# Kernel tuning notes

Hardware: AMD Instinct MI355X
Metric: run time of the kernel (lower is better)

## Reference

```python
import jax, jax.numpy as jnp
import numpy as np
import math

B, S, H = 8, 1024, 1024
NUM_LABELS = 2

# torch nn.Linear weight [out,in]; we store transposed [in,out] so y = x @ W + b

def _mha(x, mask, qw, qb, kw, kb, vw, vb, ow, ob, n_heads):
    b, s, h = x.shape
    d = h // n_heads
    Q = (x @ qw + qb).reshape(b, s, n_heads, d)
    K = (x @ kw + kb).reshape(b, s, n_heads, d)
    V = (x @ vw + vb).reshape(b, s, n_heads, d)
    scores = jnp.einsum('bqhd,bkhd->bhqk', Q, K) / math.sqrt(d)  # [b,h,s,s]
    if mask is not None:
        scores = jnp.where(mask[:, None, None, :] == 0, jnp.asarray(-1e9, scores.dtype), scores)
    w = jax.nn.softmax(scores, axis=-1)  # dropout is identity in eval mode
    ctx = jnp.einsum('bhqk,bkhd->bqhd', w, V).reshape(b, s, h)
    return ctx @ ow + ob, w


def _linear_params(key, fin, fout):
    k1, k2 = jax.random.split(key)
    lim = 1.0 / math.sqrt(fin)
    w = jax.random.uniform(k1, (fin, fout), jnp.float32, -lim, lim)
    b = jax.random.uniform(k2, (fout,), jnp.float32, -lim, lim)
    return w, b


def setup_inputs() -> dict:
    key = jax.random.key(0)
    ks = jax.random.split(key, 20)
    inp = {
        'hidden_states': jax.random.normal(ks[0], (B, S, H), jnp.float32),
        'attention_mask': jax.random.randint(ks[1], (B, S), 0, 2, jnp.int32),
    }
    i = 2
    for pre in ('beh', 'tmp', 'pat'):
        for nm in ('q', 'k', 'v', 'o'):
            w, b = _linear_params(ks[i], H, H)
            inp[f'{pre}_{nm}w'] = w
            inp[f'{pre}_{nm}b'] = b
            i += 1
    inp['fus1_w'], inp['fus1_b'] = _linear_params(ks[i], 3 * H, H); i += 1
    inp['fus2_w'], inp['fus2_b'] = _linear_params(ks[i], H, H // 2); i += 1
    inp['cls_w'], inp['cls_b'] = _linear_params(ks[i], H // 2, NUM_LABELS)
    return inp


def reference(hidden_states, attention_mask,
              beh_qw, beh_qb, beh_kw, beh_kb, beh_vw, beh_vb, beh_ow, beh_ob,
              tmp_qw, tmp_qb, tmp_kw, tmp_kb, tmp_vw, tmp_vb, tmp_ow, tmp_ob,
              pat_qw, pat_qb, pat_kw, pat_kb, pat_vw, pat_vb, pat_ow, pat_ob,
              fus1_w, fus1_b, fus2_w, fus2_b, cls_w, cls_b):
    beh_out, _ = _mha(hidden_states, attention_mask, beh_qw, beh_qb, beh_kw, beh_kb, beh_vw, beh_vb, beh_ow, beh_ob, 8)
    tmp_out, _ = _mha(hidden_states, attention_mask, tmp_qw, tmp_qb, tmp_kw, tmp_kb, tmp_vw, tmp_vb, tmp_ow, tmp_ob, 4)
    pat_out, _ = _mha(hidden_states, attention_mask, pat_qw, pat_qb, pat_kw, pat_kb, pat_vw, pat_vb, pat_ow, pat_ob, 4)
    m = attention_mask[:, :, None].astype(hidden_states.dtype)  # [B,S,1]
    denom = m.sum(axis=1)  # [B,1] broadcast like torch expand_as sum
    beh_p = (beh_out * m).sum(axis=1) / denom
    tmp_p = (tmp_out * m).sum(axis=1) / denom
    pat_p = (pat_out * m).sum(axis=1) / denom
    fused = jnp.concatenate([beh_p, tmp_p, pat_p], axis=-1)  # [B,3H]
    h1 = jax.nn.relu(fused @ fus1_w + fus1_b)
    h2 = jax.nn.relu(h1 @ fus2_w + fus2_b)
    logits = h2 @ cls_w + cls_b
    return logits
```

## Files before the change

### kernel.cpp

```cpp
#include <hip/hip_runtime.h>

#define DEVINL __device__ __forceinline__
typedef __attribute__((ext_vector_type(8))) __bf16 bf16x8;
typedef __attribute__((ext_vector_type(4))) __bf16 bf16x4;
typedef __attribute__((ext_vector_type(4))) float f32x4;

DEVINL void gload16(void* lds, const void* g) {
  __builtin_amdgcn_global_load_lds((const __attribute__((address_space(1))) void*)g,
                                   (__attribute__((address_space(3))) void*)lds, 16, 0, 0);
}

__global__ void cvt_bf16_kernel(const float* __restrict__ in, __bf16* __restrict__ out, int n4) {
  int i = blockIdx.x * 256 + threadIdx.x;
  if (i >= n4) return;
  float4 v = reinterpret_cast<const float4*>(in)[i];
  bf16x4 o;
  o.x = (__bf16)v.x; o.y = (__bf16)v.y; o.z = (__bf16)v.z; o.w = (__bf16)v.w;
  reinterpret_cast<bf16x4*>(out)[i] = o;
}

__global__ void wt_pack_kernel(const float* __restrict__ Wq, const float* __restrict__ Wk,
                               const float* __restrict__ Wv, __bf16* __restrict__ WT) {
  __shared__ float t[64][65];
  int k0 = blockIdx.x * 64;
  int n0 = blockIdx.y * 64;
  const float* W = (n0 < 1024) ? Wq : (n0 < 2048 ? Wk : Wv);
  int nn0 = n0 & 1023;
  int r = threadIdx.x >> 6, c = threadIdx.x & 63;
#pragma unroll
  for (int i = 0; i < 16; ++i)
    t[r + i*4][c] = W[(size_t)(k0 + r + i*4) * 1024 + nn0 + c];
  __syncthreads();
#pragma unroll
  for (int i = 0; i < 16; ++i) {
    int row = r + i*4;
    WT[(size_t)(n0 + row) * 1024 + k0 + c] = (__bf16)t[c][row];
  }
}

__global__ __launch_bounds__(256) void gemm_qkv_kernel(
    const __bf16* __restrict__ A, const __bf16* __restrict__ WT,
    const float* __restrict__ bq, const float* __restrict__ bk, const float* __restrict__ bv,
    __bf16* __restrict__ C) {
  constexpr int N_ = 3072, K_ = 1024;
  __shared__ __align__(16) __bf16 lds[2][(128 + 128) * 64];
  int tid = threadIdx.x;
  int lane = tid & 63;
  int wave = tid >> 6;
  int l15 = lane & 15, l4 = lane >> 4;
  int wr = wave >> 1, wc = wave & 1;
  int n0 = blockIdx.x * 128, m0 = blockIdx.y * 128;

  f32x4 acc[4][4] = {};

  const char* Abase = (const char*)(A  + (size_t)m0 * K_);
  const char* Bbase = (const char*)(WT + (size_t)n0 * K_);

  auto STAGE = [&](int buf, int kt) {
    char* Al = (char*)lds[buf];
    char* Bl = (char*)(lds[buf] + 128 * 64);
#pragma unroll
    for (int i = 0; i < 4; ++i) {
      int c = i * 256 + tid;
      int r = c >> 3, cc = c & 7, g = cc ^ (r & 7);
      gload16(Al + (size_t)(c & ~63) * 16,
              Abase + (size_t)r * (K_ * 2) + kt * 128 + g * 16);
      gload16(Bl + (size_t)(c & ~63) * 16,
              Bbase + (size_t)r * (K_ * 2) + kt * 128 + g * 16);
    }
  };

  int cur = 0;
  STAGE(0, 0);
  for (int kt = 0; kt < 16; ++kt) {
    if (kt < 15) {
      STAGE(cur ^ 1, kt + 1);
      asm volatile("s_waitcnt vmcnt(8)" ::: "memory");
    } else {
      asm volatile("s_waitcnt vmcnt(0)" ::: "memory");
    }
    __builtin_amdgcn_s_barrier();
    const char* Al = (const char*)lds[cur];
    const char* Bl = (const char*)(lds[cur] + 128 * 64);
#pragma unroll
    for (int kk = 0; kk < 2; ++kk) {
      bf16x8 af[4], bfr[4];
      int j = kk * 4 + l4;
#pragma unroll
      for (int m = 0; m < 4; ++m) {
        int row = wr * 64 + m * 16 + l15;
        af[m] = *(const bf16x8*)(Al + ((size_t)row * 8 + (j ^ (row & 7))) * 16);
      }
#pragma unroll
      for (int n = 0; n < 4; ++n) {
        int row = wc * 64 + n * 16 + l15;
        bfr[n] = *(const bf16x8*)(Bl + ((size_t)row * 8 + (j ^ (row & 7))) * 16);
      }
      __builtin_amdgcn_s_setprio(1);
#pragma unroll
      for (int m = 0; m < 4; ++m)
#pragma unroll
        for (int n = 0; n < 4; ++n)
          acc[m][n] = __builtin_amdgcn_mfma_f32_16x16x32_bf16(af[m], bfr[n], acc[m][n], 0, 0, 0);
      __builtin_amdgcn_s_setprio(0);
    }
    __builtin_amdgcn_s_barrier();
    cur ^= 1;
  }

#pragma unroll
  for (int n = 0; n < 4; ++n) {
    int col = n0 + wc * 64 + n * 16 + l15;
    const float* bias = (col < 1024) ? bq : (col < 2048 ? bk : bv);
    float bv_ = bias[col & 1023];
#pragma unroll
    for (int m = 0; m < 4; ++m) {
      int rowb = m0 + wr * 64 + m * 16 + l4 * 4;
#pragma unroll
      for (int r = 0; r < 4; ++r)
        C[(size_t)(rowb + r) * N_ + col] = (__bf16)(acc[m][n][r] + bv_);
    }
  }
}

__global__ void vt_pack_kernel(const __bf16* __restrict__ QKV, __bf16* __restrict__ Vt,
                               int hcnt, int D) {
  __shared__ __bf16 t[64][65];
  int s0 = blockIdx.x * 64, d0 = blockIdx.y * 64;
  int bh = blockIdx.z;
  int b = bh / hcnt, h = bh - b*hcnt;
  int r = threadIdx.x >> 6, c = threadIdx.x & 63;
  const __bf16* src = QKV + (size_t)b*1024*3072 + 2048 + (size_t)h*D;
#pragma unroll
  for (int i = 0; i < 16; ++i)
    t[r + i*4][c] = src[(size_t)(s0 + r + i*4)*3072 + d0 + c];
  __syncthreads();
  __bf16* dst = Vt + ((size_t)bh*D + d0)*1024 + s0;
#pragma unroll
  for (int i = 0; i < 16; ++i) {
    int row = r + i*4;
    dst[(size_t)row*1024 + c] = t[c][row];
  }
}

template<int D, int WQ, int HCNT>
__global__ __launch_bounds__(256) void attn_kernel(
    const __bf16* __restrict__ QKV, const __bf16* __restrict__ Vt,
    const int* __restrict__ mask, float* __restrict__ ctx) {
  constexpr int QT  = 4*WQ;
  constexpr int MT  = WQ/16;
  constexpr int KC  = D/32;
  constexpr int NT2 = D/16;
  constexpr int CPR = D/8;
  __shared__ __align__(16) __bf16 smem[64*D + D*64 + 4*WQ*72];
  __shared__ float Ml[64];
  __bf16* Kl = smem;
  __bf16* Vl = smem + 64*D;
  __bf16* Pl = smem + 128*D;

  int tid = threadIdx.x;
  int lane = tid & 63, wave = tid >> 6;
  int l15 = lane & 15, l4 = lane >> 4;
  int q0 = blockIdx.x * QT;
  int h = blockIdx.y, b = blockIdx.z;
  int bh = b*HCNT + h;
  const float scale = (D == 128) ? 0.08838834764831845f : 0.0625f;

  {
    const char* qbase = (const char*)(QKV + (size_t)(b*1024 + q0)*3072 + (size_t)h*D);
    for (int c0 = 0; c0 < QT*D/8; c0 += 256) {
      int c = c0 + tid;
      int row = c / CPR, cc = c % CPR;
      gload16((char*)smem + (c0 + (tid & ~63))*16,
              qbase + (size_t)row*6144 + ((cc ^ (row & 7))*16));
    }
  }
  __syncthreads();
  bf16x8 qf[MT][KC];
#pragma unroll
  for (int m = 0; m < MT; ++m)
#pragma unroll
    for (int kc = 0; kc < KC; ++kc) {
      int row = wave*WQ + m*16 + l15;
      int boff = ((kc*32 + l4*8)*2) ^ ((row & 7) << 4);
      qf[m][kc] = *(const bf16x8*)((const char*)smem + (size_t)row*(D*2) + boff);
    }
  __syncthreads();

  f32x4 ao[MT][NT2] = {};
  float dsum[MT][4] = {};

  const char* kbase = (const char*)(QKV + (size_t)(b*1024)*3072 + 1024 + (size_t)h*D);
  const char* vbase = (const char*)(Vt + (size_t)bh*D*1024);

  for (int t = 0; t < 16; ++t) {
    for (int c0 = 0; c0 < 8*D; c0 += 256) {
      int c = c0 + tid;
      int row = c / CPR, cc = c % CPR;
      gload16((char*)Kl + (c0 + (tid & ~63))*16,
              kbase + (size_t)(t*64 + row)*6144 + ((cc ^ (row & 7))*16));
    }
    for (int c0 = 0; c0 < 8*D; c0 += 256) {
      int c = c0 + tid;
      int row = c >> 3, cc = c & 7;
      gload16((char*)Vl + (c0 + (tid & ~63))*16,
              vbase + (size_t)row*2048 + t*128 + ((cc ^ (row & 7))*16));
    }
    if (tid < 64) Ml[tid] = (float)mask[b*1024 + t*64 + tid];
    __syncthreads();

#pragma unroll
    for (int n = 0; n < 4; ++n) {
      f32x4 s[MT] = {};
#pragma unroll
      for (int kc = 0; kc < KC; ++kc) {
        int krow = n*16 + l15;
        int boff = ((kc*32 + l4*8)*2) ^ ((krow & 7) << 4);
        bf16x8 kf = *(const bf16x8*)((const char*)Kl + (size_t)krow*(D*2) + boff);
#pragma unroll
        for (int m = 0; m < MT; ++m)
          s[m] = __builtin_amdgcn_mfma_f32_16x16x32_bf16(qf[m][kc], kf, s[m], 0, 0, 0);
      }
      float mv = Ml[n*16 + l15];
#pragma unroll
      for (int m = 0; m < MT; ++m)
#pragma unroll
        for (int r = 0; r < 4; ++r) {
          float pf_ = __expf(s[m][r] * scale) * mv;
          __bf16 pb = (__bf16)pf_;
          dsum[m][r] += (float)pb;
          Pl[(size_t)(wave*WQ + m*16 + l4*4 + r)*72 + n*16 + l15] = pb;
        }
    }
    bf16x8 pfr[MT][2];
#pragma unroll
    for (int m = 0; m < MT; ++m)
#pragma unroll
      for (int kk = 0; kk < 2; ++kk)
        pfr[m][kk] = *(const bf16x8*)(Pl + (size_t)(wave*WQ + m*16 + l15)*72 + kk*32 + l4*8);
#pragma unroll
    for (int n2 = 0; n2 < NT2; ++n2) {
      bf16x8 vf[2];
#pragma unroll
      for (int kk = 0; kk < 2; ++kk) {
        int vrow = n2*16 + l15;
        int boff = ((kk*32 + l4*8)*2) ^ ((vrow & 7) << 4);
        vf[kk] = *(const bf16x8*)((const char*)Vl + (size_t)vrow*128 + boff);
      }
#pragma unroll
      for (int m = 0; m < MT; ++m)
#pragma unroll
        for (int kk = 0; kk < 2; ++kk)
          ao[m][n2] = __builtin_amdgcn_mfma_f32_16x16x32_bf16(pfr[m][kk], vf[kk], ao[m][n2], 0, 0, 0);
    }
    __syncthreads();
  }

  float inv[MT][4];
#pragma unroll
  for (int m = 0; m < MT; ++m)
#pragma unroll
    for (int r = 0; r < 4; ++r) {
      float v = dsum[m][r];
      v += __shfl_xor(v, 1, 64);
      v += __shfl_xor(v, 2, 64);
      v += __shfl_xor(v, 4, 64);
      v += __shfl_xor(v, 8, 64);
      inv[m][r] = 1.0f / v;
    }
#pragma unroll
  for (int m = 0; m < MT; ++m) {
    int rowb = b*1024 + q0 + wave*WQ + m*16 + l4*4;
#pragma unroll
    for (int n2 = 0; n2 < NT2; ++n2) {
      int col = h*D + n2*16 + l15;
#pragma unroll
      for (int r = 0; r < 4; ++r)
        ctx[(size_t)(rowb + r)*1024 + col] = ao[m][n2][r] * inv[m][r];
    }
  }
}

__global__ void denom_kernel(const int* __restrict__ mask, float* __restrict__ denom) {
  int b = blockIdx.x, t = threadIdx.x;
  int acc = 0;
  for (int s = t; s < 1024; s += 256) acc += mask[b*1024 + s];
  for (int o = 32; o; o >>= 1) acc += __shfl_down(acc, o, 64);
  __shared__ int red[4];
  if ((t & 63) == 0) red[t >> 6] = acc;
  __syncthreads();
  if (t == 0) denom[b] = (float)(red[0] + red[1] + red[2] + red[3]);
}

__global__ void pool_partial_kernel(const float* __restrict__ ctx, const int* __restrict__ mask,
                                    float* __restrict__ part) {
  int sc = blockIdx.x;
  int b  = blockIdx.y;
  int t  = threadIdx.x;
  const float* base = ctx + (size_t)b*1024*1024 + (size_t)sc*32*1024;
  const int* mrow = mask + b*1024 + sc*32;
  float4 acc = {0.f, 0.f, 0.f, 0.f};
  for (int s = 0; s < 32; ++s) {
    if (mrow[s]) {
      float4 v = reinterpret_cast<const float4*>(base + (size_t)s*1024)[t];
      acc.x += v.x; acc.y += v.y; acc.z += v.z; acc.w += v.w;
    }
  }
  reinterpret_cast<float4*>(part + ((size_t)b*32 + sc)*1024)[t] = acc;
}

__global__ void pool_reduce_kernel(const float* __restrict__ part, const float* __restrict__ denom,
                                   float* __restrict__ out) {
  int i = blockIdx.x*256 + threadIdx.x;
  int b = i >> 10, c = i & 1023;
  float a = 0.f;
#pragma unroll
  for (int sc = 0; sc < 32; ++sc) a += part[((size_t)b*32 + sc)*1024 + c];
  out[i] = a / denom[b];
}

__global__ void oproj_partial_kernel(const float* __restrict__ pooled,
    const float* __restrict__ W0, const float* __restrict__ W1, const float* __restrict__ W2,
    float* __restrict__ part) {
  int ai = blockIdx.z;
  const float* W = (ai == 0) ? W0 : (ai == 1 ? W1 : W2);
  int ks = blockIdx.y, k0 = ks*128;
  __shared__ float xl[8*128];
  const float* P = pooled + ai*8192;
  for (int i = threadIdx.x; i < 8*128; i += 256) {
    int b = i >> 7, kk = i & 127;
    xl[i] = P[b*1024 + k0 + kk];
  }
  __syncthreads();
  int n = blockIdx.x*256 + threadIdx.x;
  float acc[8] = {};
  for (int kk = 0; kk < 128; ++kk) {
    float w = W[(size_t)(k0+kk)*1024 + n];
#pragma unroll
    for (int b = 0; b < 8; ++b) acc[b] += xl[b*128 + kk] * w;
  }
#pragma unroll
  for (int b = 0; b < 8; ++b) part[(((size_t)ai*8 + ks)*8 + b)*1024 + n] = acc[b];
}

__global__ void oproj_reduce_kernel(const float* __restrict__ part,
    const float* __restrict__ b0, const float* __restrict__ b1, const float* __restrict__ b2,
    float* __restrict__ fused) {
  int i = blockIdx.x*256 + threadIdx.x;
  int ai = i >> 13, rem = i & 8191;
  int b = rem >> 10, n = rem & 1023;
  const float* bb = (ai == 0) ? b0 : (ai == 1 ? b1 : b2);
  float a = bb[n];
#pragma unroll
  for (int ks = 0; ks < 8; ++ks) a += part[(((size_t)ai*8 + ks)*8 + b)*1024 + n];
  fused[b*3072 + ai*1024 + n] = a;
}

__global__ void fc_partial_kernel(const float* __restrict__ X, const float* __restrict__ W,
                                  float* __restrict__ part, int Kin, int Nout, int kchunk) {
  extern __shared__ float xl[];
  int ks = blockIdx.y, k0 = ks*kchunk;
  for (int i = threadIdx.x; i < 8*kchunk; i += 256) {
    int b = i / kchunk, kk = i - b*kchunk;
    xl[i] = X[b*Kin + k0 + kk];
  }
  __syncthreads();
  int n = blockIdx.x*256 + threadIdx.x;
  float acc[8] = {};
  for (int kk = 0; kk < kchunk; ++kk) {
    float w = W[(size_t)(k0+kk)*Nout + n];
#pragma unroll
    for (int b = 0; b < 8; ++b) acc[b] += xl[b*kchunk + kk] * w;
  }
#pragma unroll
  for (int b = 0; b < 8; ++b) part[((size_t)ks*8 + b)*Nout + n] = acc[b];
}

__global__ void fc_reduce_kernel(const float* __restrict__ part, const float* __restrict__ bias,
                                 float* __restrict__ out, int Nout, int KS, int do_relu) {
  int i = blockIdx.x*256 + threadIdx.x;
  int b = i / Nout, n = i - b*Nout;
  float a = bias[n];
  for (int ks = 0; ks < KS; ++ks) a += part[((size_t)ks*8 + b)*Nout + n];
  out[i] = do_relu ? fmaxf(a, 0.f) : a;
}

__global__ void cls_kernel(const float* __restrict__ h2, const float* __restrict__ W,
                           const float* __restrict__ bias, float* __restrict__ out) {
  int t = threadIdx.x;
  int o = t >> 4, sl = t & 15;
  int b = o >> 1, n = o & 1;
  float a = 0.f;
  for (int k = sl; k < 512; k += 16) a += h2[b*512 + k] * W[k*2 + n];
#pragma unroll
  for (int m = 1; m < 16; m <<= 1) a += __shfl_xor(a, m, 64);
  if (sl == 0) out[o] = a + bias[n];
}

extern "C" void kernel_launch(void* const* d_in, const int* in_sizes, int n_in,
                              void* d_out, int out_size, void* d_ws, size_t ws_size,
                              hipStream_t stream) {
  const float* X   = (const float*)d_in[0];
  const int* mask  = (const int*)d_in[1];
  const float* w_[3][8];
  for (int a = 0; a < 3; ++a)
    for (int j = 0; j < 8; ++j)
      w_[a][j] = (const float*)d_in[2 + a*8 + j];
  const float* fus1_w = (const float*)d_in[26];
  const float* fus1_b = (const float*)d_in[27];
  const float* fus2_w = (const float*)d_in[28];
  const float* fus2_b = (const float*)d_in[29];
  const float* cls_w  = (const float*)d_in[30];
  const float* cls_b  = (const float*)d_in[31];

  char* p = (char*)d_ws;
  auto carve = [&](size_t bytes) { char* r = p; p += (bytes + 255) & ~(size_t)255; return r; };
  __bf16* Xb    = (__bf16*)carve((size_t)8192*1024*2);
  __bf16* WTb   = (__bf16*)carve((size_t)3072*1024*2);
  __bf16* QKVb  = (__bf16*)carve((size_t)8192*3072*2);
  __bf16* Vtb   = (__bf16*)carve((size_t)8192*1024*2);
  float* ctxb   = (float*)carve((size_t)8192*1024*4);
  float* pooledb= (float*)carve(3*8*1024*4);
  float* denomb = (float*)carve(256);
  float* fusedb = (float*)carve(8*3072*4);
  float* partb  = (float*)carve((size_t)24*8*1024*4);
  float* opartb = (float*)carve((size_t)3*8*8*1024*4);
  float* poolpartb = (float*)carve((size_t)8*32*1024*4);
  float* h1b    = (float*)carve(8*1024*4);
  float* h2b    = (float*)carve(8*512*4);
  if ((size_t)(p - (char*)d_ws) > ws_size) return;

  cvt_bf16_kernel<<<8192, 256, 0, stream>>>(X, Xb, 8192*1024/4);
  denom_kernel<<<8, 256, 0, stream>>>(mask, denomb);

  for (int a = 0; a < 3; ++a) {
    wt_pack_kernel<<<dim3(16,48), 256, 0, stream>>>(w_[a][0], w_[a][2], w_[a][4], WTb);
    gemm_qkv_kernel<<<dim3(24,64), 256, 0, stream>>>(Xb, WTb, w_[a][1], w_[a][3], w_[a][5], QKVb);
    if (a == 0) {
      vt_pack_kernel<<<dim3(16,2,64), 256, 0, stream>>>(QKVb, Vtb, 8, 128);
      attn_kernel<128,32,8><<<dim3(8,8,8), 256, 0, stream>>>(QKVb, Vtb, mask, ctxb);
    } else {
      vt_pack_kernel<<<dim3(16,4,32), 256, 0, stream>>>(QKVb, Vtb, 4, 256);
      attn_kernel<256,16,4><<<dim3(16,4,8), 256, 0, stream>>>(QKVb, Vtb, mask, ctxb);
    }
    pool_partial_kernel<<<dim3(32,8), 256, 0, stream>>>(ctxb, mask, poolpartb);
    pool_reduce_kernel<<<32, 256, 0, stream>>>(poolpartb, denomb, pooledb + a*8192);
  }

  oproj_partial_kernel<<<dim3(4,8,3), 256, 0, stream>>>(pooledb,
      w_[0][6], w_[1][6], w_[2][6], opartb);
  oproj_reduce_kernel<<<96, 256, 0, stream>>>(opartb,
      w_[0][7], w_[1][7], w_[2][7], fusedb);
  fc_partial_kernel<<<dim3(4,24), 256, 8*128*4, stream>>>(fusedb, fus1_w, partb, 3072, 1024, 128);
  fc_reduce_kernel<<<32, 256, 0, stream>>>(partb, fus1_b, h1b, 1024, 24, 1);
  fc_partial_kernel<<<dim3(2,8), 256, 8*128*4, stream>>>(h1b, fus2_w, partb, 1024, 512, 128);
  fc_reduce_kernel<<<16, 256, 0, stream>>>(partb, fus2_b, h2b, 512, 8, 1);
  cls_kernel<<<1, 256, 0, stream>>>(h2b, cls_w, cls_b, (float*)d_out);
}
```

Measured before the change: 511.2 us.

## Overlap K/V tile loads with compute and remap attention blocks per XCD

Restructures the attention loop so the V tile loads during the QK^T/softmax phase and the next K tile loads during the PV phase, with barriers moved to match. The mask is read straight from global memory into registers instead of through shared memory. The grid is flattened to 1D and remapped so that all query blocks of one (batch, head) land on the same XCD, which improves L2 reuse of K/V. The added barrier and the tighter load/compute interleaving could cost some throughput if the loads do not actually hide.

```diff
diff --git a/kernel.cpp b/kernel.cpp
--- a/kernel.cpp
+++ b/kernel.cpp
@@ -148,12 +148,12 @@
     const __bf16* __restrict__ QKV, const __bf16* __restrict__ Vt,
     const int* __restrict__ mask, float* __restrict__ ctx) {
   constexpr int QT  = 4*WQ;
+  constexpr int QB  = 1024/QT;
   constexpr int MT  = WQ/16;
   constexpr int KC  = D/32;
   constexpr int NT2 = D/16;
   constexpr int CPR = D/8;
   __shared__ __align__(16) __bf16 smem[64*D + D*64 + 4*WQ*72];
-  __shared__ float Ml[64];
   __bf16* Kl = smem;
   __bf16* Vl = smem + 64*D;
   __bf16* Pl = smem + 128*D;
@@ -161,9 +161,12 @@
   int tid = threadIdx.x;
   int lane = tid & 63, wave = tid >> 6;
   int l15 = lane & 15, l4 = lane >> 4;
-  int q0 = blockIdx.x * QT;
-  int h = blockIdx.y, b = blockIdx.z;
-  int bh = b*HCNT + h;
+  int d = blockIdx.x;
+  int xcd = d & 7, j = d >> 3;
+  int qb = j % QB, g = j / QB;
+  int p = g*8 + xcd;
+  int h = p % HCNT, b = p / HCNT;
+  int q0 = qb * QT;
   const float scale = (D == 128) ? 0.08838834764831845f : 0.0625f;
 
   {
@@ -191,23 +194,33 @@
   float dsum[MT][4] = {};
 
   const char* kbase = (const char*)(QKV + (size_t)(b*1024)*3072 + 1024 + (size_t)h*D);
-  const char* vbase = (const char*)(Vt + (size_t)bh*D*1024);
-
-  for (int t = 0; t < 16; ++t) {
+  const char* vbase = (const char*)(Vt + (size_t)(b*HCNT + h)*D*1024);
+
+  auto STAGE_K = [&](int t) {
     for (int c0 = 0; c0 < 8*D; c0 += 256) {
       int c = c0 + tid;
       int row = c / CPR, cc = c % CPR;
       gload16((char*)Kl + (c0 + (tid & ~63))*16,
               kbase + (size_t)(t*64 + row)*6144 + ((cc ^ (row & 7))*16));
     }
+  };
+  auto STAGE_V = [&](int t) {
     for (int c0 = 0; c0 < 8*D; c0 += 256) {
       int c = c0 + tid;
       int row = c >> 3, cc = c & 7;
       gload16((char*)Vl + (c0 + (tid & ~63))*16,
               vbase + (size_t)row*2048 + t*128 + ((cc ^ (row & 7))*16));
     }
-    if (tid < 64) Ml[tid] = (float)mask[b*1024 + t*64 + tid];
+  };
+
+  STAGE_K(0);
+  for (int t = 0; t < 16; ++t) {
     __syncthreads();
+    STAGE_V(t);
+    float mv[4];
+#pragma unroll
+    for (int n = 0; n < 4; ++n)
+      mv[n] = (float)mask[b*1024 + t*64 + n*16 + l15];
 
 #pragma unroll
     for (int n = 0; n < 4; ++n) {
@@ -221,17 +234,19 @@
         for (int m = 0; m < MT; ++m)
           s[m] = __builtin_amdgcn_mfma_f32_16x16x32_bf16(qf[m][kc], kf, s[m], 0, 0, 0);
       }
-      float mv = Ml[n*16 + l15];
 #pragma unroll
       for (int m = 0; m < MT; ++m)
 #pragma unroll
         for (int r = 0; r < 4; ++r) {
-          float pf_ = __expf(s[m][r] * scale) * mv;
+          float pf_ = __expf(s[m][r] * scale) * mv[n];
           __bf16 pb = (__bf16)pf_;
           dsum[m][r] += (float)pb;
           Pl[(size_t)(wave*WQ + m*16 + l4*4 + r)*72 + n*16 + l15] = pb;
         }
     }
+    __syncthreads();
+    if (t < 15) STAGE_K(t + 1);
+
     bf16x8 pfr[MT][2];
 #pragma unroll
     for (int m = 0; m < MT; ++m)
@@ -253,7 +268,6 @@
         for (int kk = 0; kk < 2; ++kk)
           ao[m][n2] = __builtin_amdgcn_mfma_f32_16x16x32_bf16(pfr[m][kk], vf[kk], ao[m][n2], 0, 0, 0);
     }
-    __syncthreads();
   }
 
   float inv[MT][4];
@@ -438,10 +452,10 @@
     gemm_qkv_kernel<<<dim3(24,64), 256, 0, stream>>>(Xb, WTb, w_[a][1], w_[a][3], w_[a][5], QKVb);
     if (a == 0) {
       vt_pack_kernel<<<dim3(16,2,64), 256, 0, stream>>>(QKVb, Vtb, 8, 128);
-      attn_kernel<128,32,8><<<dim3(8,8,8), 256, 0, stream>>>(QKVb, Vtb, mask, ctxb);
+      attn_kernel<128,32,8><<<512, 256, 0, stream>>>(QKVb, Vtb, mask, ctxb);
     } else {
       vt_pack_kernel<<<dim3(16,4,32), 256, 0, stream>>>(QKVb, Vtb, 4, 256);
-      attn_kernel<256,16,4><<<dim3(16,4,8), 256, 0, stream>>>(QKVb, Vtb, mask, ctxb);
+      attn_kernel<256,16,4><<<512, 256, 0, stream>>>(QKVb, Vtb, mask, ctxb);
     }
     pool_partial_kernel<<<dim3(32,8), 256, 0, stream>>>(ctxb, mask, poolpartb);
     pool_reduce_kernel<<<32, 256, 0, stream>>>(poolpartb, denomb, pooledb + a*8192);
```

Measured after the change: 502.7 us. No clear change (-1.7%).
